# Kernel optimization log

Measured on AMD Instinct MI355X. Metric: run time of the kernel, lower is better.

Reference implementation:

```python
import jax, jax.numpy as jnp
import numpy as np

VOCAB, D_MODEL, DICT, TOP_K = 50257, 512, 16384, 32
N_CONCEPTS, N_RELATIONS = 16, 6
B, S = 1024, 32


def sparse_topk(coeffs, top_k):
    # abs-topk along last dim, keep signed values, scatter to dense
    _, idx = jax.lax.top_k(jnp.abs(coeffs), top_k)          # [B, k]
    signed = jnp.take_along_axis(coeffs, idx, axis=-1)      # [B, k]
    rows = jnp.arange(coeffs.shape[0])[:, None]
    return jnp.zeros_like(coeffs).at[rows, idx].set(signed)


def setup_inputs() -> dict:
    key = jax.random.key(0)
    ks = jax.random.split(key, 16)
    f = lambda k, shape, scale: jax.random.normal(k, shape, dtype=jnp.float32) * scale
    inp = {
        'clean_tokens': jax.random.randint(ks[0], (B, S), 0, VOCAB),
        'noisy_tokens': jax.random.randint(ks[1], (B, S), 0, VOCAB),
        'embedding': f(ks[2], (VOCAB, D_MODEL), 1.0),
        'enc_w1': f(ks[3], (D_MODEL, D_MODEL), D_MODEL ** -0.5),
        'enc_b1': jnp.zeros((D_MODEL,), jnp.float32),
        'enc_w2': f(ks[4], (D_MODEL, D_MODEL), D_MODEL ** -0.5),
        'enc_b2': jnp.zeros((D_MODEL,), jnp.float32),
        'shared_atoms': f(ks[5], (DICT, D_MODEL), 0.04),
        'router_w': f(ks[6], (DICT, D_MODEL), D_MODEL ** -0.5),
        'concept_delta_w': f(ks[7], (DICT, D_MODEL), D_MODEL ** -0.5),
        'relation_delta_w': f(ks[8], (DICT, D_MODEL), D_MODEL ** -0.5),
        'concept_head_w': f(ks[9], (N_CONCEPTS, D_MODEL), D_MODEL ** -0.5),
        'concept_head_b': jnp.zeros((N_CONCEPTS,), jnp.float32),
        'relation_head_w': f(ks[10], (N_RELATIONS, D_MODEL), D_MODEL ** -0.5),
        'relation_head_b': jnp.zeros((N_RELATIONS,), jnp.float32),
    }
    return inp


def reference(clean_tokens, noisy_tokens, embedding, enc_w1, enc_b1, enc_w2, enc_b2,
              shared_atoms, router_w, concept_delta_w, relation_delta_w,
              concept_head_w, concept_head_b, relation_head_w, relation_head_b):
    def pooled(tokens):
        x = embedding[tokens].mean(axis=1)                       # [B, D]
        h = jax.nn.silu(x @ enc_w1.T + enc_b1)
        return h @ enc_w2.T + enc_b2

    def encode(p, delta_w):
        coeffs = p @ router_w.T + 0.3 * (p @ delta_w.T)          # [B, DICT]
        sparse = sparse_topk(coeffs, TOP_K)
        rep = sparse @ shared_atoms                              # [B, D]
        return rep, sparse

    clean_p = pooled(clean_tokens)
    noisy_p = pooled(noisy_tokens)
    c_rep, c_sp = encode(clean_p, concept_delta_w)
    r_rep, r_sp = encode(clean_p, relation_delta_w)
    nc_rep, nc_sp = encode(noisy_p, concept_delta_w)
    nr_rep, nr_sp = encode(noisy_p, relation_delta_w)

    fused_clean = 0.2 * clean_p + 0.9 * c_rep + 0.9 * r_rep
    fused_noisy = 0.2 * noisy_p + 0.9 * nc_rep + 0.9 * nr_rep

    return (fused_clean @ concept_head_w.T + concept_head_b,
            fused_clean @ relation_head_w.T + relation_head_b,
            fused_noisy @ concept_head_w.T + concept_head_b,
            fused_noisy @ relation_head_w.T + relation_head_b,
            c_sp, r_sp, nc_sp, nr_sp)
```

## Files before the change

kernel.cpp:

```cpp
#include <hip/hip_runtime.h>


typedef _Float16 f16x8 __attribute__((ext_vector_type(8)));
typedef _Float16 f16x4 __attribute__((ext_vector_type(4)));
typedef float f32x4 __attribute__((ext_vector_type(4)));

#define OUT_SPARSE 45056
#define SPARSE_PER 16777216

#define ASYNC16(gp, lp) __builtin_amdgcn_global_load_lds(                      \
    (const __attribute__((address_space(1))) void*)(gp),                       \
    (__attribute__((address_space(3))) void*)(lp), 16, 0, 0)

__global__ __launch_bounds__(128) void pool_kernel(
    const int* __restrict__ ct, const int* __restrict__ nt,
    const float* __restrict__ emb, double* __restrict__ xout)
{
    const int row = blockIdx.x, s = blockIdx.y;
    const int tid = threadIdx.x;
    __shared__ int tk[32];
    const int* t = (s ? nt : ct) + row * 32;
    if (tid < 32) tk[tid] = t[tid];
    __syncthreads();
    const int d = tid * 4;
    double a0 = 0, a1 = 0, a2 = 0, a3 = 0;
    for (int i = 0; i < 32; ++i) {
        const float4 v = *(const float4*)(emb + (size_t)tk[i] * 512 + d);
        a0 += (double)v.x; a1 += (double)v.y; a2 += (double)v.z; a3 += (double)v.w;
    }
    double* o = xout + ((size_t)s * 1024 + row) * 512 + d;
    o[0] = a0 * 0.03125; o[1] = a1 * 0.03125; o[2] = a2 * 0.03125; o[3] = a3 * 0.03125;
}

__global__ __launch_bounds__(256) void enc_gemm(
    const double* __restrict__ A, const float* __restrict__ W,
    const float* __restrict__ bias, double* __restrict__ C,
    _Float16* __restrict__ C16, int act)
{
    __shared__ double Ask[16][68];
    __shared__ double Wsk[16][68];
    const int tid = threadIdx.x;
    const int m0 = blockIdx.y * 64, n0 = blockIdx.x * 64;
    const int ty = tid >> 4, tx = tid & 15;
    const int r = tid >> 2, c4 = (tid & 3) * 4;
    double acc[4][4] = {};
    for (int k0 = 0; k0 < 512; k0 += 16) {
        const double4 av = *(const double4*)(A + (size_t)(m0 + r) * 512 + k0 + c4);
        const float4  wv = *(const float4*) (W + (size_t)(n0 + r) * 512 + k0 + c4);
        __syncthreads();
        Ask[c4 + 0][r] = av.x; Ask[c4 + 1][r] = av.y; Ask[c4 + 2][r] = av.z; Ask[c4 + 3][r] = av.w;
        Wsk[c4 + 0][r] = (double)wv.x; Wsk[c4 + 1][r] = (double)wv.y;
        Wsk[c4 + 2][r] = (double)wv.z; Wsk[c4 + 3][r] = (double)wv.w;
        __syncthreads();
#pragma unroll
        for (int k = 0; k < 16; ++k) {
            const double4 a = *(const double4*)&Ask[k][ty * 4];
            const double4 b = *(const double4*)&Wsk[k][tx * 4];
            const double aa[4] = {a.x, a.y, a.z, a.w};
            const double bb[4] = {b.x, b.y, b.z, b.w};
#pragma unroll
            for (int i = 0; i < 4; ++i)
#pragma unroll
                for (int j = 0; j < 4; ++j) acc[i][j] += aa[i] * bb[j];
        }
    }
#pragma unroll
    for (int i = 0; i < 4; ++i) {
        const int row = m0 + ty * 4 + i;
#pragma unroll
        for (int j = 0; j < 4; ++j) {
            const int col = n0 + tx * 4 + j;
            double v = acc[i][j] + (double)bias[col];
            if (act) v = v / (1.0 + exp(-v));
            C[(size_t)row * 512 + col] = v;
            if (C16) C16[(size_t)row * 512 + col] = (_Float16)v;
        }
    }
}

__global__ __launch_bounds__(256) void combine_kernel(
    const float* __restrict__ router, const float* __restrict__ cd,
    const float* __restrict__ rd, _Float16* __restrict__ wc,
    _Float16* __restrict__ wr, float* __restrict__ wcf,
    float* __restrict__ wrf)
{
    const size_t i = ((size_t)blockIdx.x * 256 + threadIdx.x) * 4;
    if (i >= (size_t)16384 * 512) return;
    const float4 r = *(const float4*)(router + i);
    const float4 c = *(const float4*)(cd + i);
    const float4 d = *(const float4*)(rd + i);
    const float4 fc = { r.x + 0.3f * c.x, r.y + 0.3f * c.y, r.z + 0.3f * c.z, r.w + 0.3f * c.w };
    const float4 fr = { r.x + 0.3f * d.x, r.y + 0.3f * d.y, r.z + 0.3f * d.z, r.w + 0.3f * d.w };
    f16x4 hc = { (_Float16)fc.x, (_Float16)fc.y, (_Float16)fc.z, (_Float16)fc.w };
    f16x4 hr = { (_Float16)fr.x, (_Float16)fr.y, (_Float16)fr.z, (_Float16)fr.w };
    *(f16x4*)(wc + i) = hc;
    *(f16x4*)(wr + i) = hr;
    *(float4*)(wcf + i) = fc;
    *(float4*)(wrf + i) = fr;
}

__global__ __launch_bounds__(256) void approx_gemm(
    const _Float16* __restrict__ P, const _Float16* __restrict__ Wc,
    const _Float16* __restrict__ Wr, unsigned* __restrict__ candg)
{
    __shared__ _Float16 As[8192];
    __shared__ _Float16 Bs[8192];
    __shared__ float    ssp[128][2];
    __shared__ unsigned cutk_s[128];
    __shared__ unsigned ecnt[128];

    const int tid = threadIdx.x;
    const int q = blockIdx.z;
    const int n0 = blockIdx.x * 128, m0 = blockIdx.y * 128;
    const _Float16* Agbl = P + (size_t)(q >> 1) * 524288;
    const _Float16* Bgbl = (q & 1) ? Wr : Wc;

    const int lane = tid & 63, w = tid >> 6;
    const int wm = w & 1, wn = w >> 1;
    const int lr = lane & 15, lk = lane >> 4;
    const int xr = lr & 7;

    const int srow = lane >> 3;
    const int cg = (lane & 7) ^ srow;
    const _Float16* ag[4];
    const _Float16* bg[4];
    _Float16* al[4];
    _Float16* bl[4];
#pragma unroll
    for (int i = 0; i < 4; ++i) {
        const int G = i * 4 + w;
        const int rr0 = G * 8 + srow;
        ag[i] = Agbl + (size_t)(m0 + rr0) * 512 + cg * 8;
        bg[i] = Bgbl + (size_t)(n0 + rr0) * 512 + cg * 8;
        al[i] = As + G * 512;
        bl[i] = Bs + G * 512;
    }

    const f32x4 zero = {0.f, 0.f, 0.f, 0.f};
    f32x4 acc[4][4];
#pragma unroll
    for (int i = 0; i < 4; ++i)
#pragma unroll
        for (int j = 0; j < 4; ++j) acc[i][j] = zero;

    for (int kt = 0; kt < 8; ++kt) {
        const int k0 = kt * 64;
        __syncthreads();
#pragma unroll
        for (int i = 0; i < 4; ++i) ASYNC16(ag[i] + k0, al[i]);
#pragma unroll
        for (int i = 0; i < 4; ++i) ASYNC16(bg[i] + k0, bl[i]);
        __syncthreads();
#pragma unroll
        for (int kk = 0; kk < 2; ++kk) {
            f16x8 af[4], bf[4];
#pragma unroll
            for (int i = 0; i < 4; ++i)
                af[i] = *(const f16x8*)(As + (wm * 64 + i * 16 + lr) * 64 + (((kk << 2) | lk) ^ xr) * 8);
#pragma unroll
            for (int j = 0; j < 4; ++j)
                bf[j] = *(const f16x8*)(Bs + (wn * 64 + j * 16 + lr) * 64 + (((kk << 2) | lk) ^ xr) * 8);
#pragma unroll
            for (int i = 0; i < 4; ++i)
#pragma unroll
                for (int j = 0; j < 4; ++j)
                    acc[i][j] = __builtin_amdgcn_mfma_f32_16x16x32_f16(af[i], bf[j], acc[i][j], 0, 0, 0);
        }
    }

    if (tid < 128) ecnt[tid] = 0;
#pragma unroll
    for (int i = 0; i < 4; ++i)
#pragma unroll
        for (int rr = 0; rr < 4; ++rr) {
            float s = 0.f;
#pragma unroll
            for (int j = 0; j < 4; ++j) { const float v = acc[i][j][rr]; s = fmaf(v, v, s); }
            s += __shfl_xor(s, 1); s += __shfl_xor(s, 2);
            s += __shfl_xor(s, 4); s += __shfl_xor(s, 8);
            if (lr == 0) ssp[wm * 64 + i * 16 + lk * 4 + rr][wn] = s;
        }
    __syncthreads();
    if (tid < 128) {
        const float sig2 = (ssp[tid][0] + ssp[tid][1]) * (1.f / 128.f);
        const _Float16 hc = (_Float16)(2.0f * sqrtf(sig2));
        cutk_s[tid] = (unsigned)__builtin_bit_cast(unsigned short, hc) & 0x7FFFu;
    }
    __syncthreads();

    unsigned* emit = (unsigned*)As;
#pragma unroll
    for (int i = 0; i < 4; ++i)
#pragma unroll
        for (int rr = 0; rr < 4; ++rr) {
            const int row = wm * 64 + i * 16 + lk * 4 + rr;
            const unsigned ck = cutk_s[row];
#pragma unroll
            for (int j = 0; j < 4; ++j) {
                const float v = acc[i][j][rr];
                const _Float16 hv = (_Float16)v;
                const unsigned key = (unsigned)__builtin_bit_cast(unsigned short, hv) & 0x7FFFu;
                if (key >= ck && key) {
                    const unsigned pos = atomicAdd(&ecnt[row], 1u);
                    const int col = n0 + wn * 64 + j * 16 + lr;
                    if (pos < 32u) emit[row * 32 + pos] = (key << 16) | (unsigned)(16383 - col);
                }
            }
        }
    __syncthreads();
    {
        const int r2 = tid >> 1, h2 = tid & 1;
        const unsigned c = min(ecnt[r2], 32u);
#pragma unroll
        for (int s2 = 0; s2 < 16; ++s2) {
            const unsigned sl = (unsigned)(h2 * 16 + s2);
            if (sl >= c) emit[r2 * 32 + sl] = 0u;
        }
        unsigned* eg = candg + (((size_t)q * 1024 + m0 + r2) * 128 + blockIdx.x) * 32;
        const uint4* e4 = (const uint4*)(emit + r2 * 32 + h2 * 16);
        uint4* g4 = (uint4*)(eg + h2 * 16);
        g4[0] = e4[0]; g4[1] = e4[1]; g4[2] = e4[2]; g4[3] = e4[3];
    }
}

__global__ __launch_bounds__(256) void select_kernel(
    const double* __restrict__ pw, const float* __restrict__ wcf,
    const float* __restrict__ wrf, const unsigned* __restrict__ candg,
    const float* __restrict__ atoms, float* __restrict__ selvw,
    int* __restrict__ seliw, float* __restrict__ repw)
{
    constexpr int NCAP = 160, NRE = 64;
    const int row = blockIdx.x, q = blockIdx.y;
    const int pset = q >> 1;
    const int tid = threadIdx.x;

    __shared__ unsigned hist[1024];
    __shared__ unsigned pscan[256];
    __shared__ double prow[512];
    __shared__ unsigned cent[NCAP];
    __shared__ int r64i[NRE];
    __shared__ double cval[NRE];
    __shared__ float selv[32];
    __shared__ int seli[32];
    __shared__ int cnt, bstar;

    const double* prg = pw + ((size_t)pset * 1024 + row) * 512;
    const unsigned* crow = candg + ((size_t)q * 1024 + row) * 4096;

    for (int b = tid; b < 1024; b += 256) hist[b] = 0;
    if (tid == 0) { cnt = 0; bstar = -1; }
    if (tid < NRE) r64i[tid] = 0;
    prow[tid] = prg[tid];
    prow[tid + 256] = prg[tid + 256];

    uint4 cv[4];
#pragma unroll
    for (int p = 0; p < 4; ++p) cv[p] = ((const uint4*)crow)[p * 256 + tid];
    __syncthreads();

#pragma unroll
    for (int p = 0; p < 4; ++p) {
        const unsigned ee[4] = {cv[p].x, cv[p].y, cv[p].z, cv[p].w};
#pragma unroll
        for (int e = 0; e < 4; ++e)
            if (ee[e]) atomicAdd(&hist[ee[e] >> 21], 1u);
    }
    __syncthreads();

    const unsigned h0 = hist[tid * 4], h1 = hist[tid * 4 + 1];
    const unsigned h2 = hist[tid * 4 + 2], h3 = hist[tid * 4 + 3];
    const unsigned l3 = h3, l2 = h2 + l3, l1 = h1 + l2, l0 = h0 + l1;
    pscan[tid] = l0;
    __syncthreads();
    for (int s = 1; s < 256; s <<= 1) {
        const unsigned v = (tid + s < 256) ? pscan[tid + s] : 0u;
        __syncthreads();
        pscan[tid] += v;
        __syncthreads();
    }
    {
        const unsigned above = (tid < 255) ? pscan[tid + 1] : 0u;
        int best = -1;
        if (l0 + above >= 64u) best = tid * 4;
        if (l1 + above >= 64u) best = tid * 4 + 1;
        if (l2 + above >= 64u) best = tid * 4 + 2;
        if (l3 + above >= 64u) best = tid * 4 + 3;
        if (best >= 0) atomicMax(&bstar, best);
    }
    __syncthreads();
    const unsigned kmin = (unsigned)(bstar < 0 ? 1 : bstar) << 5;

#pragma unroll
    for (int p = 0; p < 4; ++p) {
        const unsigned ee[4] = {cv[p].x, cv[p].y, cv[p].z, cv[p].w};
#pragma unroll
        for (int e = 0; e < 4; ++e) {
            if (ee[e] && (ee[e] >> 16) >= kmin) {
                const int pos = atomicAdd(&cnt, 1);
                if (pos < NCAP) cent[pos] = ee[e];
            }
        }
    }
    __syncthreads();
    const int nc = min(cnt, NCAP);

    for (int p = tid; p < nc; p += 256) {
        const unsigned e = cent[p];
        int rr = 0;
        for (int j = 0; j < nc; ++j) rr += (cent[j] > e) ? 1 : 0;
        if (rr < NRE) r64i[rr] = 16383 - (int)(e & 0xFFFFu);
    }
    __syncthreads();

    const float* wsel = (q & 1) ? wrf : wcf;
    const int w = tid >> 6, lane = tid & 63;
    for (int c = w; c < NRE; c += 4) {
        const int idx = r64i[c];
        const float4* rp4 = (const float4*)(wsel + (size_t)idx * 512);
        const float4 r0 = rp4[lane * 2], r1 = rp4[lane * 2 + 1];
        const double* pv = prow + lane * 8;
        double aR = pv[0] * (double)r0.x + pv[1] * (double)r0.y + pv[2] * (double)r0.z + pv[3] * (double)r0.w
                  + pv[4] * (double)r1.x + pv[5] * (double)r1.y + pv[6] * (double)r1.z + pv[7] * (double)r1.w;
        for (int sh = 32; sh > 0; sh >>= 1) aR += __shfl_down(aR, sh);
        if (lane == 0) cval[c] = aR;
    }
    __syncthreads();

    if (tid < NRE) {
        const double av = fabs(cval[tid]);
        const int mi = r64i[tid];
        int rr = 0;
        for (int j = 0; j < NRE; ++j) {
            const double aj = fabs(cval[j]);
            rr += (aj > av || (aj == av && r64i[j] < mi)) ? 1 : 0;
        }
        if (rr < 32) { selv[rr] = (float)cval[tid]; seli[rr] = mi; }
    }
    __syncthreads();
    if (tid < 32) {
        const size_t sb = ((size_t)q * 1024 + row) * 32 + tid;
        selvw[sb] = selv[tid];
        seliw[sb] = seli[tid];
    }

    double a0 = 0, a1 = 0;
    for (int k = 0; k < 32; ++k) {
        const double v = (double)selv[k];
        const float* ar = atoms + (size_t)seli[k] * 512;
        a0 += v * (double)ar[tid];
        a1 += v * (double)ar[tid + 256];
    }
    float* rp = repw + ((size_t)q * 1024 + row) * 512;
    rp[tid] = (float)a0;
    rp[tid + 256] = (float)a1;
}

__global__ __launch_bounds__(256) void heads_kernel(
    const double* __restrict__ pw, const float* __restrict__ repw,
    const float* __restrict__ chw, const float* __restrict__ chb,
    const float* __restrict__ rhw, const float* __restrict__ rhb,
    const float* __restrict__ selvw, const int* __restrict__ seliw,
    float* __restrict__ out)
{
    const int row = blockIdx.x, s = blockIdx.y;
    const int tid = threadIdx.x;
    __shared__ double fused[512];

    float4* z0 = (float4*)(out + (size_t)OUT_SPARSE + (size_t)(2 * s + 0) * SPARSE_PER + (size_t)row * 16384);
    float4* z1 = (float4*)(out + (size_t)OUT_SPARSE + (size_t)(2 * s + 1) * SPARSE_PER + (size_t)row * 16384);
    const float4 z = {0.f, 0.f, 0.f, 0.f};
#pragma unroll
    for (int i = 0; i < 16; ++i) { z0[i * 256 + tid] = z; z1[i * 256 + tid] = z; }

    const double* pr = pw + ((size_t)s * 1024 + row) * 512;
    const float* rc = repw + ((size_t)(s * 2 + 0) * 1024 + row) * 512;
    const float* rr = repw + ((size_t)(s * 2 + 1) * 1024 + row) * 512;
    for (int d = tid; d < 512; d += 256)
        fused[d] = 0.2 * pr[d] + 0.9 * (double)rc[d] + 0.9 * (double)rr[d];
    __syncthreads();

    if (tid < 64) {
        const int qq = s * 2 + (tid >> 5), k = tid & 31;
        const size_t sb = ((size_t)qq * 1024 + row) * 32 + k;
        out[(size_t)OUT_SPARSE + (size_t)qq * SPARSE_PER + (size_t)row * 16384 + (size_t)seliw[sb]] = selvw[sb];
    }

    const int w = tid >> 6, lane = tid & 63;
    for (int o = w; o < 22; o += 4) {
        const float* hw2 = (o < 16) ? (chw + (size_t)o * 512) : (rhw + (size_t)(o - 16) * 512);
        double acc = 0;
#pragma unroll
        for (int j = 0; j < 8; ++j) acc += fused[lane + 64 * j] * (double)hw2[lane + 64 * j];
        for (int sh = 32; sh > 0; sh >>= 1) acc += __shfl_down(acc, sh);
        if (lane == 0) {
            if (o < 16) out[(s ? 22528 : 0) + row * 16 + o] = (float)(acc + (double)chb[o]);
            else        out[(s ? 38912 : 16384) + row * 6 + (o - 16)] = (float)(acc + (double)rhb[o - 16]);
        }
    }
}

extern "C" void kernel_launch(void* const* d_in, const int* in_sizes, int n_in,
                              void* d_out, int out_size, void* d_ws, size_t ws_size,
                              hipStream_t stream)
{
    const int*   ctok   = (const int*)d_in[0];
    const int*   ntok   = (const int*)d_in[1];
    const float* emb    = (const float*)d_in[2];
    const float* w1     = (const float*)d_in[3];
    const float* b1     = (const float*)d_in[4];
    const float* w2     = (const float*)d_in[5];
    const float* b2     = (const float*)d_in[6];
    const float* atoms  = (const float*)d_in[7];
    const float* router = (const float*)d_in[8];
    const float* cdelta = (const float*)d_in[9];
    const float* rdelta = (const float*)d_in[10];
    const float* chw    = (const float*)d_in[11];
    const float* chb    = (const float*)d_in[12];
    const float* rhw    = (const float*)d_in[13];
    const float* rhb    = (const float*)d_in[14];
    float* out = (float*)d_out;

    float*    wcf   = out + OUT_SPARSE;
    float*    wrf   = wcf + 8388608;
    unsigned* candg = (unsigned*)(wrf + 8388608);

    double*    xw   = (double*)d_ws;
    double*    hw   = xw + 1048576;
    double*    pw   = hw + 1048576;
    float*     repw = (float*)(pw + 1048576);
    _Float16*  pf16 = (_Float16*)(repw + 2097152);
    _Float16*  wcw  = pf16 + 1048576;
    _Float16*  wrw  = wcw + 8388608;
    float*     selvw = (float*)hw;
    int*       seliw = (int*)(selvw + 131072);

    pool_kernel<<<dim3(1024, 2), 128, 0, stream>>>(ctok, ntok, emb, xw);
    enc_gemm<<<dim3(8, 32), 256, 0, stream>>>(xw, w1, b1, hw, (_Float16*)nullptr, 1);
    enc_gemm<<<dim3(8, 32), 256, 0, stream>>>(hw, w2, b2, pw, pf16, 0);
    combine_kernel<<<8192, 256, 0, stream>>>(router, cdelta, rdelta, wcw, wrw, wcf, wrf);
    approx_gemm<<<dim3(128, 8, 4), 256, 0, stream>>>(pf16, wcw, wrw, candg);
    select_kernel<<<dim3(1024, 4), 256, 0, stream>>>(pw, wcf, wrf, candg, atoms, selvw, seliw, repw);
    heads_kernel<<<dim3(1024, 2), 256, 0, stream>>>(pw, repw, chw, chb, rhw, rhb, selvw, seliw, out);
}
```

Baseline: 873.0 us.

## Load GEMM fragments directly from global memory instead of staging through LDS

The approx_gemm kernel no longer stages A/B tiles in shared memory through async global-to-LDS loads with barriers. Each lane now loads its MFMA fragments straight from global memory into registers, so both in-loop __syncthreads go away and LDS use drops to the emit buffer, allowing a launch bound of 4 blocks per CU. In exchange, tiles that several waves share are re-read from global memory or L2 with no LDS reuse, and the per-lane loads are strided rows that coalesce less well.

```diff
diff --git a/kernel.cpp b/kernel.cpp
--- a/kernel.cpp
+++ b/kernel.cpp
@@ -7,10 +7,6 @@
 
 #define OUT_SPARSE 45056
 #define SPARSE_PER 16777216
-
-#define ASYNC16(gp, lp) __builtin_amdgcn_global_load_lds(                      \
-    (const __attribute__((address_space(1))) void*)(gp),                       \
-    (__attribute__((address_space(3))) void*)(lp), 16, 0, 0)
 
 __global__ __launch_bounds__(128) void pool_kernel(
     const int* __restrict__ ct, const int* __restrict__ nt,
@@ -99,12 +95,11 @@
     *(float4*)(wrf + i) = fr;
 }
 
-__global__ __launch_bounds__(256) void approx_gemm(
+__global__ __launch_bounds__(256, 4) void approx_gemm(
     const _Float16* __restrict__ P, const _Float16* __restrict__ Wc,
     const _Float16* __restrict__ Wr, unsigned* __restrict__ candg)
 {
-    __shared__ _Float16 As[8192];
-    __shared__ _Float16 Bs[8192];
+    __shared__ unsigned emit[128 * 32];
     __shared__ float    ssp[128][2];
     __shared__ unsigned cutk_s[128];
     __shared__ unsigned ecnt[128];
@@ -118,22 +113,13 @@
     const int lane = tid & 63, w = tid >> 6;
     const int wm = w & 1, wn = w >> 1;
     const int lr = lane & 15, lk = lane >> 4;
-    const int xr = lr & 7;
-
-    const int srow = lane >> 3;
-    const int cg = (lane & 7) ^ srow;
-    const _Float16* ag[4];
-    const _Float16* bg[4];
-    _Float16* al[4];
-    _Float16* bl[4];
+
+    const _Float16* ap[4];
+    const _Float16* bp[4];
 #pragma unroll
     for (int i = 0; i < 4; ++i) {
-        const int G = i * 4 + w;
-        const int rr0 = G * 8 + srow;
-        ag[i] = Agbl + (size_t)(m0 + rr0) * 512 + cg * 8;
-        bg[i] = Bgbl + (size_t)(n0 + rr0) * 512 + cg * 8;
-        al[i] = As + G * 512;
-        bl[i] = Bs + G * 512;
+        ap[i] = Agbl + (size_t)(m0 + wm * 64 + i * 16 + lr) * 512 + lk * 8;
+        bp[i] = Bgbl + (size_t)(n0 + wn * 64 + i * 16 + lr) * 512 + lk * 8;
     }
 
     const f32x4 zero = {0.f, 0.f, 0.f, 0.f};
@@ -144,28 +130,25 @@
         for (int j = 0; j < 4; ++j) acc[i][j] = zero;
 
     for (int kt = 0; kt < 8; ++kt) {
-        const int k0 = kt * 64;
-        __syncthreads();
-#pragma unroll
-        for (int i = 0; i < 4; ++i) ASYNC16(ag[i] + k0, al[i]);
-#pragma unroll
-        for (int i = 0; i < 4; ++i) ASYNC16(bg[i] + k0, bl[i]);
-        __syncthreads();
-#pragma unroll
-        for (int kk = 0; kk < 2; ++kk) {
-            f16x8 af[4], bf[4];
-#pragma unroll
-            for (int i = 0; i < 4; ++i)
-                af[i] = *(const f16x8*)(As + (wm * 64 + i * 16 + lr) * 64 + (((kk << 2) | lk) ^ xr) * 8);
+        f16x8 a0[4], a1[4], b0[4], b1[4];
+#pragma unroll
+        for (int i = 0; i < 4; ++i) {
+            a0[i] = *(const f16x8*)(ap[i]);
+            a1[i] = *(const f16x8*)(ap[i] + 32);
+            b0[i] = *(const f16x8*)(bp[i]);
+            b1[i] = *(const f16x8*)(bp[i] + 32);
+            ap[i] += 64; bp[i] += 64;
+        }
+#pragma unroll
+        for (int i = 0; i < 4; ++i)
 #pragma unroll
             for (int j = 0; j < 4; ++j)
-                bf[j] = *(const f16x8*)(Bs + (wn * 64 + j * 16 + lr) * 64 + (((kk << 2) | lk) ^ xr) * 8);
-#pragma unroll
-            for (int i = 0; i < 4; ++i)
-#pragma unroll
-                for (int j = 0; j < 4; ++j)
-                    acc[i][j] = __builtin_amdgcn_mfma_f32_16x16x32_f16(af[i], bf[j], acc[i][j], 0, 0, 0);
-        }
+                acc[i][j] = __builtin_amdgcn_mfma_f32_16x16x32_f16(a0[i], b0[j], acc[i][j], 0, 0, 0);
+#pragma unroll
+        for (int i = 0; i < 4; ++i)
+#pragma unroll
+            for (int j = 0; j < 4; ++j)
+                acc[i][j] = __builtin_amdgcn_mfma_f32_16x16x32_f16(a1[i], b1[j], acc[i][j], 0, 0, 0);
     }
 
     if (tid < 128) ecnt[tid] = 0;
@@ -188,7 +171,6 @@
     }
     __syncthreads();
 
-    unsigned* emit = (unsigned*)As;
 #pragma unroll
     for (int i = 0; i < 4; ++i)
 #pragma unroll
```

Result: slower. 969.5 us (+11.1%).
